# Kernel tuning notes

Hardware: AMD Instinct MI355X
Metric: run time of the kernel (lower is better)

The kernel has to match this reference:

```python
import jax, jax.numpy as jnp
import numpy as np

EPS = 1e-5


def _ln(t):
    # Custom LayerNorm from the source: unbiased variance (torch.var default),
    # gamma=ones, beta=zeros (plain tensors, never trained) -> plain normalize.
    m = t.mean(axis=-1, keepdims=True)
    v = t.var(axis=-1, keepdims=True, ddof=1)
    return (t - m) / jnp.sqrt(v + EPS)


def setup_inputs() -> dict:
    key = jax.random.key(0)
    B, T, C, H = 4, 2048, 1024, 16
    hs = C // H
    ks = jax.random.split(key, 10)
    s_in = (1.0 / C) ** 0.5   # nn.Linear default init scale (approx, uniform->normal ok for ref)
    s_ff = (1.0 / (4 * C)) ** 0.5
    return {
        "x": jax.random.normal(ks[0], (B, T, C), jnp.float32),
        "Wq": jax.random.normal(ks[1], (H, C, hs), jnp.float32) * s_in,
        "Wk": jax.random.normal(ks[2], (H, C, hs), jnp.float32) * s_in,
        "Wv": jax.random.normal(ks[3], (H, C, hs), jnp.float32) * s_in,
        "Wo": jax.random.normal(ks[4], (C, C), jnp.float32) * s_in,
        "bo": jnp.zeros((C,), jnp.float32),
        "W1": jax.random.normal(ks[5], (C, 4 * C), jnp.float32) * s_in,
        "b1": jnp.zeros((4 * C,), jnp.float32),
        "W2": jax.random.normal(ks[6], (4 * C, C), jnp.float32) * s_ff,
        "b2": jnp.zeros((C,), jnp.float32),
    }


def reference(x, Wq, Wk, Wv, Wo, bo, W1, b1, W2, b2):
    B, T, C = x.shape
    H, _, hs = Wq.shape
    # per-head projections (equivalent to the Python loop over Head modules)
    q = jnp.einsum('btc,hcd->bhtd', x, Wq)
    k = jnp.einsum('btc,hcd->bhtd', x, Wk)
    v = jnp.einsum('btc,hcd->bhtd', x, Wv)
    scores = jnp.einsum('bhtd,bhsd->bhts', q, k) * (hs ** -0.5)
    causal = jnp.tril(jnp.ones((T, T), dtype=bool))
    scores = jnp.where(causal, scores, jnp.float32(-jnp.inf))
    w = jax.nn.softmax(scores, axis=-1)          # dropout is identity in eval
    o = jnp.einsum('bhts,bhsd->bhtd', w, v)
    o = o.transpose(0, 2, 1, 3).reshape(B, T, C)  # concat heads
    attn = o @ Wo + bo
    x1 = x + _ln(attn)
    ff = jax.nn.relu(x1 @ W1 + b1) @ W2 + b2
    return x1 + _ln(ff)
```

## Files before the change

### kernel.cpp

```cpp
#include <hip/hip_runtime.h>
#include <hip/hip_bf16.h>

using bf16 = __hip_bfloat16;
typedef __attribute__((ext_vector_type(8))) short s8v;
typedef __attribute__((ext_vector_type(4))) float f4v;
typedef __attribute__((ext_vector_type(16))) float f16v;
typedef __attribute__((ext_vector_type(4))) unsigned int u4v;

#define QSCALE 0.18033688011112042f

__device__ __forceinline__ void gld_lds16(const void* g, void* l) {
  __builtin_amdgcn_global_load_lds(
      (const __attribute__((address_space(1))) void*)g,
      (__attribute__((address_space(3))) void*)l, 16, 0, 0);
}

__device__ __forceinline__ unsigned short bfbits(float f) {
  bf16 t = __float2bfloat16(f);
  return *reinterpret_cast<unsigned short*>(&t);
}

__device__ __forceinline__ unsigned int pk2(float lo, float hi) {
  return (unsigned int)bfbits(lo) | ((unsigned int)bfbits(hi) << 16);
}

__device__ __forceinline__ void lswap(unsigned int& a, unsigned int& b) {
  asm("v_permlane32_swap_b32 %0, %1" : "+v"(a), "+v"(b));
}

__global__ __launch_bounds__(256) void f32_to_bf16_k(const float* __restrict__ in,
                                                     bf16* __restrict__ out, size_t n) {
  const size_t i = ((size_t)blockIdx.x * 256 + threadIdx.x) * 4;
  if (i + 3 < n) {
    const float4 v = *(const float4*)(in + i);
    out[i + 0] = __float2bfloat16(v.x);
    out[i + 1] = __float2bfloat16(v.y);
    out[i + 2] = __float2bfloat16(v.z);
    out[i + 3] = __float2bfloat16(v.w);
  }
}

__global__ __launch_bounds__(256) void tr_to_bf16_k(const float* __restrict__ in,
                                                    bf16* __restrict__ out,
                                                    int R, int C,
                                                    size_t inb, size_t outb) {
  __shared__ float tile[32][33];
  in  += (size_t)blockIdx.z * inb;
  out += (size_t)blockIdx.z * outb;
  const int r0 = blockIdx.y * 32, c0 = blockIdx.x * 32;
  const int tx = threadIdx.x & 31, ty = threadIdx.x >> 5;
#pragma unroll
  for (int i = 0; i < 4; ++i)
    tile[ty + i * 8][tx] = in[(size_t)(r0 + ty + i * 8) * C + c0 + tx];
  __syncthreads();
#pragma unroll
  for (int i = 0; i < 4; ++i)
    out[(size_t)(c0 + ty + i * 8) * R + r0 + tx] = __float2bfloat16(tile[tx][ty + i * 8]);
}

template <int MODE>
__global__ __launch_bounds__(256, 2) void gemm_bt(const bf16* __restrict__ A,
                                                  const bf16* __restrict__ B,
                                                  const float* __restrict__ bias,
                                                  float* __restrict__ Cf,
                                                  bf16* __restrict__ Cb,
                                                  bf16* __restrict__ Vout,
                                                  int M, int N, int K) {
  __shared__ __attribute__((aligned(16))) bf16 As[128 * 32];
  __shared__ __attribute__((aligned(16))) bf16 Bs[128 * 32];
  const int tid  = threadIdx.x;
  const int wid  = tid >> 6;
  const int lane = tid & 63;
  const int quad = lane >> 4;
  const int l16  = lane & 15;
  const int bm = blockIdx.y * 128;
  const int bn = blockIdx.x * 128;
  const int wm = (wid >> 1) * 64;
  const int wn = (wid & 1) * 64;

  f4v acc[4][4];
#pragma unroll
  for (int i = 0; i < 4; ++i)
#pragma unroll
    for (int j = 0; j < 4; ++j) acc[i][j] = (f4v){0.f, 0.f, 0.f, 0.f};

  const bf16* Ag = A + (size_t)(bm + wid * 32 + (lane >> 2)) * K + (lane & 3) * 8;
  const bf16* Bg = B + (size_t)(bn + wid * 32 + (lane >> 2)) * K + (lane & 3) * 8;
  bf16* AsW = As + wid * 32 * 32;
  bf16* BsW = Bs + wid * 32 * 32;

  for (int k0 = 0; k0 < K; k0 += 32) {
    __syncthreads();
    gld_lds16(Ag,                  AsW);
    gld_lds16(Ag + (size_t)16 * K, AsW + 16 * 32);
    gld_lds16(Bg,                  BsW);
    gld_lds16(Bg + (size_t)16 * K, BsW + 16 * 32);
    Ag += 32; Bg += 32;
    __syncthreads();

    s8v af[4], bfr[4];
#pragma unroll
    for (int mi = 0; mi < 4; ++mi)
      af[mi] = *(const s8v*)(As + (wm + mi * 16 + l16) * 32 + quad * 8);
#pragma unroll
    for (int ni = 0; ni < 4; ++ni)
      bfr[ni] = *(const s8v*)(Bs + (wn + ni * 16 + l16) * 32 + quad * 8);
#pragma unroll
    for (int mi = 0; mi < 4; ++mi)
#pragma unroll
      for (int ni = 0; ni < 4; ++ni)
        acc[mi][ni] = __builtin_amdgcn_mfma_f32_16x16x32_bf16(af[mi], bfr[ni], acc[mi][ni], 0, 0, 0);
  }

  const size_t ldc = (size_t)N;
#pragma unroll
  for (int mi = 0; mi < 4; ++mi) {
#pragma unroll
    for (int ni = 0; ni < 4; ++ni) {
      const int col  = bn + wn + ni * 16 + l16;
      const int row0 = bm + wm + mi * 16 + quad * 4;
      if (MODE == 0) {
        if (col < 2048) {
          const float sc = (col < 1024) ? QSCALE : 1.0f;
#pragma unroll
          for (int r = 0; r < 4; ++r)
            Cb[(size_t)(row0 + r) * ldc + col] = __float2bfloat16(acc[mi][ni][r] * sc);
        } else {
          ushort4 pk;
          pk.x = bfbits(acc[mi][ni][0]);
          pk.y = bfbits(acc[mi][ni][1]);
          pk.z = bfbits(acc[mi][ni][2]);
          pk.w = bfbits(acc[mi][ni][3]);
          const int bb = row0 >> 11, t = row0 & 2047;
          *(ushort4*)&Vout[((size_t)(bb * 1024 + col - 2048)) * 2048 + t] = pk;
        }
      } else {
        const float bv = bias[col];
#pragma unroll
        for (int r = 0; r < 4; ++r) {
          const float v = acc[mi][ni][r] + bv;
          if (MODE == 1) Cf[(size_t)(row0 + r) * ldc + col] = v;
          else           Cb[(size_t)(row0 + r) * ldc + col] = __float2bfloat16(fmaxf(v, 0.f));
        }
      }
    }
  }
}

template <int MODE>
__global__ __launch_bounds__(512, 2) void gemm256(const bf16* __restrict__ A,
                                                  const bf16* __restrict__ B,
                                                  const float* __restrict__ bias,
                                                  float* __restrict__ Cf,
                                                  bf16* __restrict__ Cb,
                                                  bf16* __restrict__ Vout,
                                                  int M, int N, int K) {
  __shared__ __attribute__((aligned(16))) bf16 AS[2][256 * 64];
  __shared__ __attribute__((aligned(16))) bf16 BS[2][256 * 64];

  const int tid  = threadIdx.x;
  const int wid  = tid >> 6;
  const int lane = tid & 63;
  const int l16  = lane & 15;
  const int quad = lane >> 4;
  const int wm   = wid >> 2;
  const int wn   = wid & 3;

  const int gx  = gridDim.x;
  const int nwg = gx * gridDim.y;
  int lin = blockIdx.y * gx + blockIdx.x;
  lin = (lin & 7) * (nwg >> 3) + (lin >> 3);
  const int bm = (lin / gx) * 256;
  const int bn = (lin % gx) * 256;

  const int d0 = tid * 16;
  const int a0 = d0 ^ (((d0 >> 9) & 1) << 5);
  const int sr = a0 >> 7;
  const int scol = (a0 & 127) >> 1;
  const bf16* Asrc = A + (size_t)(bm + sr) * K + scol;
  const bf16* Bsrc = B + (size_t)(bn + sr) * K + scol;
  char* const AW0 = (char*)&AS[0][0] + wid * 1024;
  char* const AW1 = (char*)&AS[1][0] + wid * 1024;
  char* const BW0 = (char*)&BS[0][0] + wid * 1024;
  char* const BW1 = (char*)&BS[1][0] + wid * 1024;

  const int sq16 = (quad * 16) ^ (((l16 >> 2) & 1) << 5);
  const int rdA  = l16 * 128 + sq16;
  const int rdB  = (wn & 1) * 8192 + l16 * 128 + sq16;

#define STAGE2(dst, src) \
  do { gld_lds16((src), (dst)); gld_lds16((src) + (size_t)64 * K, (dst) + 8192); } while (0)

  f4v acc[8][4];
#pragma unroll
  for (int i = 0; i < 8; ++i)
#pragma unroll
    for (int j = 0; j < 4; ++j) acc[i][j] = (f4v){0.f, 0.f, 0.f, 0.f};

  const int NT = K >> 6;

  STAGE2(AW0,         Asrc);
  STAGE2(AW0 + 16384, Asrc + (size_t)128 * K);
  STAGE2(BW0,         Bsrc);
  STAGE2(BW0 + 16384, Bsrc + (size_t)128 * K);
  STAGE2(BW1,         Bsrc + 64);
  STAGE2(BW1 + 16384, Bsrc + (size_t)128 * K + 64);
  asm volatile("s_waitcnt vmcnt(4)" ::: "memory");
  asm volatile("s_barrier" ::: "memory");

  s8v bfrag[4][2];
  for (int u = 0; u < NT; ++u) {
    const int bsel = u & 1;
    const char* Ard = (char*)&AS[bsel][0] + wm * 16384 + rdA;
    const char* Brd = (char*)&BS[bsel][0] + (wn >> 1) * 16384 + rdB;
    char* const AWn = bsel ? AW0 : AW1;
    char* const BWc = bsel ? BW1 : BW0;
    const bf16* An = Asrc + (size_t)(u + 1) * 64;
    const bf16* Bn = Bsrc + (size_t)(u + 2) * 64;
#pragma unroll
    for (int p = 0; p < 4; ++p) {
      s8v afrag[2][2];
#pragma unroll
      for (int j = 0; j < 2; ++j)
#pragma unroll
        for (int kk = 0; kk < 2; ++kk)
          afrag[j][kk] = *(const s8v*)(Ard + (p * 2 + j) * 2048 + kk * 64);
      if (p == 0) {
#pragma unroll
        for (int nf = 0; nf < 4; ++nf)
#pragma unroll
          for (int kk = 0; kk < 2; ++kk)
            bfrag[nf][kk] = *(const s8v*)(Brd + nf * 2048 + kk * 64);
      }
      if (p == 0 && u + 1 < NT) STAGE2(AWn,         An);
      if (p == 1 && u + 1 < NT) STAGE2(AWn + 16384, An + (size_t)128 * K);
      if (p == 2 && u + 2 < NT) STAGE2(BWc,         Bn);
      if (p == 3 && u + 2 < NT) STAGE2(BWc + 16384, Bn + (size_t)128 * K);
      asm volatile("s_barrier" ::: "memory");
      asm volatile("s_waitcnt lgkmcnt(0)" ::: "memory");
      __builtin_amdgcn_sched_barrier(0);
      __builtin_amdgcn_s_setprio(1);
#pragma unroll
      for (int kk = 0; kk < 2; ++kk)
#pragma unroll
        for (int j = 0; j < 2; ++j)
#pragma unroll
          for (int nf = 0; nf < 4; ++nf)
            acc[p * 2 + j][nf] = __builtin_amdgcn_mfma_f32_16x16x32_bf16(
                afrag[j][kk], bfrag[nf][kk], acc[p * 2 + j][nf], 0, 0, 0);
      __builtin_amdgcn_s_setprio(0);
      if (p == 3) {
        if (u + 2 < NT) asm volatile("s_waitcnt vmcnt(4)" ::: "memory");
        else            asm volatile("s_waitcnt vmcnt(0)" ::: "memory");
      }
      asm volatile("s_barrier" ::: "memory");
    }
  }
#undef STAGE2

  const size_t ldc = (size_t)N;
#pragma unroll
  for (int mf = 0; mf < 8; ++mf) {
#pragma unroll
    for (int nf = 0; nf < 4; ++nf) {
      const int col  = bn + wn * 64 + nf * 16 + l16;
      const int row0 = bm + wm * 128 + mf * 16 + quad * 4;
      if (MODE == 0) {
        if (col < 2048) {
          const float sc = (col < 1024) ? QSCALE : 1.0f;
#pragma unroll
          for (int r = 0; r < 4; ++r)
            Cb[(size_t)(row0 + r) * ldc + col] = __float2bfloat16(acc[mf][nf][r] * sc);
        } else {
          ushort4 pk;
          pk.x = bfbits(acc[mf][nf][0]);
          pk.y = bfbits(acc[mf][nf][1]);
          pk.z = bfbits(acc[mf][nf][2]);
          pk.w = bfbits(acc[mf][nf][3]);
          const int bb = row0 >> 11, t = row0 & 2047;
          *(ushort4*)&Vout[((size_t)(bb * 1024 + col - 2048)) * 2048 + t] = pk;
        }
      } else {
        const float bv = bias[col];
#pragma unroll
        for (int r = 0; r < 4; ++r) {
          const float v = acc[mf][nf][r] + bv;
          if (MODE == 1) Cf[(size_t)(row0 + r) * ldc + col] = v;
          else           Cb[(size_t)(row0 + r) * ldc + col] = __float2bfloat16(fmaxf(v, 0.f));
        }
      }
    }
  }
}

__global__ __launch_bounds__(256, 3) void attn_mfma(const bf16* __restrict__ qkv,
                                                    const bf16* __restrict__ vtg,
                                                    bf16* __restrict__ o) {
  __shared__ __attribute__((aligned(16))) bf16 KsS[2][64 * 64];
  __shared__ __attribute__((aligned(16))) bf16 VtS[2][64 * 64];
  __shared__ __attribute__((aligned(16))) float tS[128];

  const int tid  = threadIdx.x;
  const int w    = tid >> 6;
  const int lane = tid & 63;
  const int l32  = lane & 31;
  const int hi   = lane >> 5;
  const int xq   = l32 & 7;

  const int lin = blockIdx.x;
  const int b = lin & 3;
  const int h = (lin >> 2) & 15;
  const int qt = 15 - (lin >> 6);

  const bf16* qbase = qkv + (size_t)b * 2048 * 3072 + h * 64;
  const bf16* kbase = qbase + 1024;
  const bf16* vbase = vtg + (size_t)(b * 1024 + h * 64) * 2048;

  const int rsub = lane >> 3;
  const int sseg = (lane & 7) ^ rsub;
  const int d0 = (w * 16) * 64;
  const int d1 = (w * 16 + 8) * 64;

  const int nkt = 2 * qt + 2;
  const int qmin_w = qt * 128 + w * 32;
  const int qmax_w = qmin_w + 31;
  const int q_lane = qmin_w + l32;

  s8v qf[4];
#pragma unroll
  for (int ks = 0; ks < 4; ++ks)
    qf[ks] = *(const s8v*)(qbase + (size_t)q_lane * 3072 + ks * 16 + hi * 8);

  float m_run = -1.0e38f, l_run = 0.f;
  f16v oacc[2];
#pragma unroll
  for (int dn = 0; dn < 2; ++dn)
#pragma unroll
    for (int r = 0; r < 16; ++r) oacc[dn][r] = 0.f;

  const bf16* kg = kbase + (size_t)(w * 16 + rsub) * 3072 + sseg * 8;
  const bf16* vg = vbase + (size_t)(w * 16 + rsub) * 2048 + sseg * 8;

  gld_lds16(kg,                    &KsS[0][d0]);
  gld_lds16(kg + (size_t)8 * 3072, &KsS[0][d1]);
  gld_lds16(vg,                    &VtS[0][d0]);
  gld_lds16(vg + (size_t)8 * 2048, &VtS[0][d1]);
  kg += (size_t)64 * 3072; vg += 64;
  __syncthreads();

  for (int kt = 0; kt < nkt; ++kt) {
    const int cb = kt & 1;

    if (kt + 1 < nkt) {
      const int nb = cb ^ 1;
      gld_lds16(kg,                    &KsS[nb][d0]);
      gld_lds16(kg + (size_t)8 * 3072, &KsS[nb][d1]);
      gld_lds16(vg,                    &VtS[nb][d0]);
      gld_lds16(vg + (size_t)8 * 2048, &VtS[nb][d1]);
      kg += (size_t)64 * 3072; vg += 64;
    }

    if (kt * 64 <= qmax_w) {
      const int kmmax = min(1, (qmax_w - kt * 64) >> 5);
      const bool diag = (kt * 64 + 63 > qmin_w);

      f16v sacc[2];
#pragma unroll
      for (int km = 0; km < 2; ++km)
#pragma unroll
        for (int r = 0; r < 16; ++r) sacc[km][r] = 0.f;

      for (int km = 0; km <= kmmax; ++km)
#pragma unroll
        for (int ks = 0; ks < 4; ++ks) {
          const s8v kf = *(const s8v*)&KsS[cb][(km * 32 + l32) * 64 +
                                               (((2 * ks + hi) ^ xq) << 3)];
          sacc[km] = __builtin_amdgcn_mfma_f32_32x32x16_bf16(kf, qf[ks], sacc[km], 0, 0, 0);
        }

      if (diag) {
        for (int km = 0; km <= kmmax; ++km)
#pragma unroll
          for (int r = 0; r < 16; ++r) {
            const int key = kt * 64 + km * 32 + (r & 3) + 8 * (r >> 2) + 4 * hi;
            if (key > q_lane) sacc[km][r] = -3.0e38f;
          }
      }

      float pmax = -3.0e38f;
#pragma unroll
      for (int km = 0; km < 2; ++km)
        if (km <= kmmax)
#pragma unroll
          for (int r = 0; r < 16; ++r) pmax = fmaxf(pmax, sacc[km][r]);
      pmax = fmaxf(pmax, __shfl_xor(pmax, 32));

      float mref = m_run;
      if (!__all(pmax <= m_run + 8.f)) {
        const float mnew = fmaxf(m_run, pmax);
        const float alpha = __builtin_amdgcn_exp2f(m_run - mnew);
        m_run = mnew; mref = mnew;
        l_run *= alpha;
        tS[w * 32 + l32] = alpha;
        f4v aF[4];
#pragma unroll
        for (int g = 0; g < 4; ++g)
          aF[g] = *(const f4v*)&tS[w * 32 + g * 8 + hi * 4];
#pragma unroll
        for (int dn = 0; dn < 2; ++dn)
#pragma unroll
          for (int r = 0; r < 16; ++r) oacc[dn][r] *= aF[r >> 2][r & 3];
      }

      float rs = 0.f;
      s8v pfr[4];
#pragma unroll
      for (int km = 0; km < 2; ++km)
        if (km <= kmmax) {
          float p[16];
#pragma unroll
          for (int r = 0; r < 16; ++r) {
            p[r] = __builtin_amdgcn_exp2f(sacc[km][r] - mref);
            rs += p[r];
          }
          unsigned int u0 = pk2(p[0], p[1]),  u1 = pk2(p[2], p[3]);
          unsigned int u2 = pk2(p[4], p[5]),  u3 = pk2(p[6], p[7]);
          lswap(u0, u2); lswap(u1, u3);
          u4v f0 = (u4v){u0, u1, u2, u3};
          pfr[2 * km] = *(s8v*)&f0;
          unsigned int v0 = pk2(p[8], p[9]),   v1 = pk2(p[10], p[11]);
          unsigned int v2 = pk2(p[12], p[13]), v3 = pk2(p[14], p[15]);
          lswap(v0, v2); lswap(v1, v3);
          u4v f1 = (u4v){v0, v1, v2, v3};
          pfr[2 * km + 1] = *(s8v*)&f1;
        }
      rs += __shfl_xor(rs, 32);
      l_run += rs;

#pragma unroll
      for (int ks = 0; ks < 4; ++ks)
        if ((ks >> 1) <= kmmax) {
#pragma unroll
          for (int dn = 0; dn < 2; ++dn) {
            const s8v vf = *(const s8v*)&VtS[cb][(dn * 32 + l32) * 64 +
                                                 (((2 * ks + hi) ^ xq) << 3)];
            oacc[dn] = __builtin_amdgcn_mfma_f32_32x32x16_bf16(pfr[ks], vf, oacc[dn], 0, 0, 0);
          }
        }
    }
    __syncthreads();
  }

  tS[w * 32 + l32] = l_run;
  f4v lF[4];
#pragma unroll
  for (int g = 0; g < 4; ++g)
    lF[g] = *(const f4v*)&tS[w * 32 + g * 8 + hi * 4];

#pragma unroll
  for (int r = 0; r < 16; ++r) {
    const float inv = __builtin_amdgcn_rcpf(lF[r >> 2][r & 3]);
    const int row = qt * 128 + w * 32 + (r & 3) + 8 * (r >> 2) + 4 * hi;
    bf16* dst = o + ((size_t)b * 2048 + row) * 1024 + h * 64 + l32;
    dst[0]  = __float2bfloat16(oacc[0][r] * inv);
    dst[32] = __float2bfloat16(oacc[1][r] * inv);
  }
}

__global__ __launch_bounds__(256) void ln_res(const float* __restrict__ xres,
                                              const float* __restrict__ t,
                                              float* __restrict__ xo,
                                              bf16* __restrict__ xob) {
  __shared__ float red[2][4];
  const int tid = threadIdx.x;
  const size_t base = (size_t)blockIdx.x * 1024;
  float v[4];
  float s = 0.f;
#pragma unroll
  for (int i = 0; i < 4; ++i) { v[i] = t[base + tid + i * 256]; s += v[i]; }
#pragma unroll
  for (int off = 32; off > 0; off >>= 1) s += __shfl_xor(s, off, 64);
  if ((tid & 63) == 0) red[0][tid >> 6] = s;
  __syncthreads();
  const float mean = (red[0][0] + red[0][1] + red[0][2] + red[0][3]) * (1.f / 1024.f);
  float ss = 0.f;
#pragma unroll
  for (int i = 0; i < 4; ++i) { const float d = v[i] - mean; ss += d * d; }
#pragma unroll
  for (int off = 32; off > 0; off >>= 1) ss += __shfl_xor(ss, off, 64);
  if ((tid & 63) == 0) red[1][tid >> 6] = ss;
  __syncthreads();
  const float var = (red[1][0] + red[1][1] + red[1][2] + red[1][3]) * (1.f / 1023.f);
  const float rstd = rsqrtf(var + 1e-5f);
#pragma unroll
  for (int i = 0; i < 4; ++i) {
    const size_t idx = base + tid + i * 256;
    const float r = xres[idx] + (v[i] - mean) * rstd;
    xo[idx] = r;
    if (xob) xob[idx] = __float2bfloat16(r);
  }
}

extern "C" void kernel_launch(void* const* d_in, const int* in_sizes, int n_in,
                              void* d_out, int out_size, void* d_ws, size_t ws_size,
                              hipStream_t stream) {
  const float* x  = (const float*)d_in[0];
  const float* Wq = (const float*)d_in[1];
  const float* Wk = (const float*)d_in[2];
  const float* Wv = (const float*)d_in[3];
  const float* Wo = (const float*)d_in[4];
  const float* bo = (const float*)d_in[5];
  const float* W1 = (const float*)d_in[6];
  const float* b1 = (const float*)d_in[7];
  const float* W2 = (const float*)d_in[8];
  const float* b2 = (const float*)d_in[9];
  float* out = (float*)d_out;

  char* ws = (char*)d_ws;
  bf16* qkv_bf = (bf16*)(ws);
  bf16* x_bf   = (bf16*)(ws + 50331648);
  bf16* WqkvT  = (bf16*)(ws + 67108864);
  bf16* WoT    = (bf16*)(ws + 73400320);
  bf16* W1T    = (bf16*)(ws + 75497472);
  bf16* W2T    = (bf16*)(ws + 83886080);
  bf16* o_bf   = (bf16*)(ws + 92274688);
  float* attn  = (float*)(ws + 109051904);
  float* x1    = (float*)(ws + 142606336);
  bf16* x1b    = (bf16*)(ws + 176160768);
  bf16* vt     = (bf16*)(ws + 192937984);
  bf16* h1     = (bf16*)(ws);
  float* ff    = (float*)(ws + 109051904);

  f32_to_bf16_k<<<8192, 256, 0, stream>>>(x, x_bf, (size_t)8388608);
  tr_to_bf16_k<<<dim3(2, 32, 16), 256, 0, stream>>>(Wq, WqkvT,               1024, 64,   65536, 65536);
  tr_to_bf16_k<<<dim3(2, 32, 16), 256, 0, stream>>>(Wk, WqkvT + 1024 * 1024, 1024, 64,   65536, 65536);
  tr_to_bf16_k<<<dim3(2, 32, 16), 256, 0, stream>>>(Wv, WqkvT + 2048 * 1024, 1024, 64,   65536, 65536);
  tr_to_bf16_k<<<dim3(32, 32, 1), 256, 0, stream>>>(Wo, WoT,                 1024, 1024, 0, 0);
  tr_to_bf16_k<<<dim3(128, 32, 1), 256, 0, stream>>>(W1, W1T,                1024, 4096, 0, 0);
  tr_to_bf16_k<<<dim3(32, 128, 1), 256, 0, stream>>>(W2, W2T,                4096, 1024, 0, 0);

  gemm256<0><<<dim3(12, 32), 512, 0, stream>>>(x_bf, WqkvT, nullptr, nullptr, qkv_bf, vt, 8192, 3072, 1024);

  attn_mfma<<<1024, 256, 0, stream>>>(qkv_bf, vt, o_bf);

  gemm_bt<1><<<dim3(8, 64), 256, 0, stream>>>(o_bf, WoT, bo, attn, nullptr, nullptr, 8192, 1024, 1024);

  ln_res<<<8192, 256, 0, stream>>>(x, attn, x1, x1b);

  gemm256<2><<<dim3(16, 32), 512, 0, stream>>>(x1b, W1T, b1, nullptr, h1, nullptr, 8192, 4096, 1024);
  gemm_bt<1><<<dim3(8, 64), 256, 0, stream>>>(h1, W2T, b2, ff, nullptr, nullptr, 8192, 1024, 4096);

  ln_res<<<8192, 256, 0, stream>>>(x1, ff, out, nullptr);
}
```

Before: 536.3 us.

## Template pipelined 256-row GEMM on N-tile and use it for N=1024 GEMMs

Makes the pipelined double-buffered 256-row GEMM generic over the N-tile width (256 or 128) and replaces the simple single-buffered 128x128 gemm_bt kernel for the Wo and W2 projections with a 256x128 instance. The intent is to bring the better software pipeline, LDS swizzle and larger M-tile to the N=1024 GEMMs, including the K=4096 FFN down-projection. The cost is fewer workgroups (256 instead of 512), which may under-fill the GPU's compute units and leave wave occupancy low.

Measured after the change: 509.8 us. 4.9% less time.

```diff
diff --git a/kernel.cpp b/kernel.cpp
--- a/kernel.cpp
+++ b/kernel.cpp
@@ -58,105 +58,18 @@
     out[(size_t)(c0 + ty + i * 8) * R + r0 + tx] = __float2bfloat16(tile[tx][ty + i * 8]);
 }
 
-template <int MODE>
-__global__ __launch_bounds__(256, 2) void gemm_bt(const bf16* __restrict__ A,
-                                                  const bf16* __restrict__ B,
-                                                  const float* __restrict__ bias,
-                                                  float* __restrict__ Cf,
-                                                  bf16* __restrict__ Cb,
-                                                  bf16* __restrict__ Vout,
-                                                  int M, int N, int K) {
-  __shared__ __attribute__((aligned(16))) bf16 As[128 * 32];
-  __shared__ __attribute__((aligned(16))) bf16 Bs[128 * 32];
-  const int tid  = threadIdx.x;
-  const int wid  = tid >> 6;
-  const int lane = tid & 63;
-  const int quad = lane >> 4;
-  const int l16  = lane & 15;
-  const int bm = blockIdx.y * 128;
-  const int bn = blockIdx.x * 128;
-  const int wm = (wid >> 1) * 64;
-  const int wn = (wid & 1) * 64;
-
-  f4v acc[4][4];
-#pragma unroll
-  for (int i = 0; i < 4; ++i)
-#pragma unroll
-    for (int j = 0; j < 4; ++j) acc[i][j] = (f4v){0.f, 0.f, 0.f, 0.f};
-
-  const bf16* Ag = A + (size_t)(bm + wid * 32 + (lane >> 2)) * K + (lane & 3) * 8;
-  const bf16* Bg = B + (size_t)(bn + wid * 32 + (lane >> 2)) * K + (lane & 3) * 8;
-  bf16* AsW = As + wid * 32 * 32;
-  bf16* BsW = Bs + wid * 32 * 32;
-
-  for (int k0 = 0; k0 < K; k0 += 32) {
-    __syncthreads();
-    gld_lds16(Ag,                  AsW);
-    gld_lds16(Ag + (size_t)16 * K, AsW + 16 * 32);
-    gld_lds16(Bg,                  BsW);
-    gld_lds16(Bg + (size_t)16 * K, BsW + 16 * 32);
-    Ag += 32; Bg += 32;
-    __syncthreads();
-
-    s8v af[4], bfr[4];
-#pragma unroll
-    for (int mi = 0; mi < 4; ++mi)
-      af[mi] = *(const s8v*)(As + (wm + mi * 16 + l16) * 32 + quad * 8);
-#pragma unroll
-    for (int ni = 0; ni < 4; ++ni)
-      bfr[ni] = *(const s8v*)(Bs + (wn + ni * 16 + l16) * 32 + quad * 8);
-#pragma unroll
-    for (int mi = 0; mi < 4; ++mi)
-#pragma unroll
-      for (int ni = 0; ni < 4; ++ni)
-        acc[mi][ni] = __builtin_amdgcn_mfma_f32_16x16x32_bf16(af[mi], bfr[ni], acc[mi][ni], 0, 0, 0);
-  }
-
-  const size_t ldc = (size_t)N;
-#pragma unroll
-  for (int mi = 0; mi < 4; ++mi) {
-#pragma unroll
-    for (int ni = 0; ni < 4; ++ni) {
-      const int col  = bn + wn + ni * 16 + l16;
-      const int row0 = bm + wm + mi * 16 + quad * 4;
-      if (MODE == 0) {
-        if (col < 2048) {
-          const float sc = (col < 1024) ? QSCALE : 1.0f;
-#pragma unroll
-          for (int r = 0; r < 4; ++r)
-            Cb[(size_t)(row0 + r) * ldc + col] = __float2bfloat16(acc[mi][ni][r] * sc);
-        } else {
-          ushort4 pk;
-          pk.x = bfbits(acc[mi][ni][0]);
-          pk.y = bfbits(acc[mi][ni][1]);
-          pk.z = bfbits(acc[mi][ni][2]);
-          pk.w = bfbits(acc[mi][ni][3]);
-          const int bb = row0 >> 11, t = row0 & 2047;
-          *(ushort4*)&Vout[((size_t)(bb * 1024 + col - 2048)) * 2048 + t] = pk;
-        }
-      } else {
-        const float bv = bias[col];
-#pragma unroll
-        for (int r = 0; r < 4; ++r) {
-          const float v = acc[mi][ni][r] + bv;
-          if (MODE == 1) Cf[(size_t)(row0 + r) * ldc + col] = v;
-          else           Cb[(size_t)(row0 + r) * ldc + col] = __float2bfloat16(fmaxf(v, 0.f));
-        }
-      }
-    }
-  }
-}
-
-template <int MODE>
-__global__ __launch_bounds__(512, 2) void gemm256(const bf16* __restrict__ A,
-                                                  const bf16* __restrict__ B,
-                                                  const float* __restrict__ bias,
-                                                  float* __restrict__ Cf,
-                                                  bf16* __restrict__ Cb,
-                                                  bf16* __restrict__ Vout,
-                                                  int M, int N, int K) {
+template <int MODE, int BN>
+__global__ __launch_bounds__(512, 2) void gemmT(const bf16* __restrict__ A,
+                                                const bf16* __restrict__ B,
+                                                const float* __restrict__ bias,
+                                                float* __restrict__ Cf,
+                                                bf16* __restrict__ Cb,
+                                                bf16* __restrict__ Vout,
+                                                int M, int N, int K) {
+  constexpr int NF = BN / 64;
+  constexpr int BH = BN / 128;
   __shared__ __attribute__((aligned(16))) bf16 AS[2][256 * 64];
-  __shared__ __attribute__((aligned(16))) bf16 BS[2][256 * 64];
+  __shared__ __attribute__((aligned(16))) bf16 BS[2][BN * 64];
 
   const int tid  = threadIdx.x;
   const int wid  = tid >> 6;
@@ -171,7 +84,7 @@
   int lin = blockIdx.y * gx + blockIdx.x;
   lin = (lin & 7) * (nwg >> 3) + (lin >> 3);
   const int bm = (lin / gx) * 256;
-  const int bn = (lin % gx) * 256;
+  const int bn = (lin % gx) * BN;
 
   const int d0 = tid * 16;
   const int a0 = d0 ^ (((d0 >> 9) & 1) << 5);
@@ -186,33 +99,39 @@
 
   const int sq16 = (quad * 16) ^ (((l16 >> 2) & 1) << 5);
   const int rdA  = l16 * 128 + sq16;
-  const int rdB  = (wn & 1) * 8192 + l16 * 128 + sq16;
-
-#define STAGE2(dst, src) \
+  const int rdB  = wn * (BN / 4) * 128 + l16 * 128 + sq16;
+
+#define STAGE_A2(dst, src) \
   do { gld_lds16((src), (dst)); gld_lds16((src) + (size_t)64 * K, (dst) + 8192); } while (0)
-
-  f4v acc[8][4];
+#define STAGE_BH(dst, src) \
+  do { gld_lds16((src), (dst)); \
+       if constexpr (BH == 2) gld_lds16((src) + (size_t)64 * K, (dst) + 8192); } while (0)
+#define WAIT_B_INFLIGHT() \
+  do { if constexpr (BN == 256) asm volatile("s_waitcnt vmcnt(4)" ::: "memory"); \
+       else                     asm volatile("s_waitcnt vmcnt(2)" ::: "memory"); } while (0)
+
+  f4v acc[8][NF];
 #pragma unroll
   for (int i = 0; i < 8; ++i)
 #pragma unroll
-    for (int j = 0; j < 4; ++j) acc[i][j] = (f4v){0.f, 0.f, 0.f, 0.f};
+    for (int j = 0; j < NF; ++j) acc[i][j] = (f4v){0.f, 0.f, 0.f, 0.f};
 
   const int NT = K >> 6;
 
-  STAGE2(AW0,         Asrc);
-  STAGE2(AW0 + 16384, Asrc + (size_t)128 * K);
-  STAGE2(BW0,         Bsrc);
-  STAGE2(BW0 + 16384, Bsrc + (size_t)128 * K);
-  STAGE2(BW1,         Bsrc + 64);
-  STAGE2(BW1 + 16384, Bsrc + (size_t)128 * K + 64);
-  asm volatile("s_waitcnt vmcnt(4)" ::: "memory");
+  STAGE_A2(AW0,         Asrc);
+  STAGE_A2(AW0 + 16384, Asrc + (size_t)128 * K);
+  STAGE_BH(BW0,             Bsrc);
+  STAGE_BH(BW0 + BH * 8192, Bsrc + (size_t)(BH * 64) * K);
+  STAGE_BH(BW1,             Bsrc + 64);
+  STAGE_BH(BW1 + BH * 8192, Bsrc + (size_t)(BH * 64) * K + 64);
+  WAIT_B_INFLIGHT();
   asm volatile("s_barrier" ::: "memory");
 
-  s8v bfrag[4][2];
+  s8v bfrag[NF][2];
   for (int u = 0; u < NT; ++u) {
     const int bsel = u & 1;
     const char* Ard = (char*)&AS[bsel][0] + wm * 16384 + rdA;
-    const char* Brd = (char*)&BS[bsel][0] + (wn >> 1) * 16384 + rdB;
+    const char* Brd = (char*)&BS[bsel][0] + rdB;
     char* const AWn = bsel ? AW0 : AW1;
     char* const BWc = bsel ? BW1 : BW0;
     const bf16* An = Asrc + (size_t)(u + 1) * 64;
@@ -227,15 +146,15 @@
           afrag[j][kk] = *(const s8v*)(Ard + (p * 2 + j) * 2048 + kk * 64);
       if (p == 0) {
 #pragma unroll
-        for (int nf = 0; nf < 4; ++nf)
+        for (int nf = 0; nf < NF; ++nf)
 #pragma unroll
           for (int kk = 0; kk < 2; ++kk)
             bfrag[nf][kk] = *(const s8v*)(Brd + nf * 2048 + kk * 64);
       }
-      if (p == 0 && u + 1 < NT) STAGE2(AWn,         An);
-      if (p == 1 && u + 1 < NT) STAGE2(AWn + 16384, An + (size_t)128 * K);
-      if (p == 2 && u + 2 < NT) STAGE2(BWc,         Bn);
-      if (p == 3 && u + 2 < NT) STAGE2(BWc + 16384, Bn + (size_t)128 * K);
+      if (p == 0 && u + 1 < NT) STAGE_A2(AWn,         An);
+      if (p == 1 && u + 1 < NT) STAGE_A2(AWn + 16384, An + (size_t)128 * K);
+      if (p == 2 && u + 2 < NT) STAGE_BH(BWc,             Bn);
+      if (p == 3 && u + 2 < NT) STAGE_BH(BWc + BH * 8192, Bn + (size_t)(BH * 64) * K);
       asm volatile("s_barrier" ::: "memory");
       asm volatile("s_waitcnt lgkmcnt(0)" ::: "memory");
       __builtin_amdgcn_sched_barrier(0);
@@ -245,25 +164,27 @@
 #pragma unroll
         for (int j = 0; j < 2; ++j)
 #pragma unroll
-          for (int nf = 0; nf < 4; ++nf)
+          for (int nf = 0; nf < NF; ++nf)
             acc[p * 2 + j][nf] = __builtin_amdgcn_mfma_f32_16x16x32_bf16(
                 afrag[j][kk], bfrag[nf][kk], acc[p * 2 + j][nf], 0, 0, 0);
       __builtin_amdgcn_s_setprio(0);
       if (p == 3) {
-        if (u + 2 < NT) asm volatile("s_waitcnt vmcnt(4)" ::: "memory");
+        if (u + 2 < NT) WAIT_B_INFLIGHT();
         else            asm volatile("s_waitcnt vmcnt(0)" ::: "memory");
       }
       asm volatile("s_barrier" ::: "memory");
     }
   }
-#undef STAGE2
+#undef STAGE_A2
+#undef STAGE_BH
+#undef WAIT_B_INFLIGHT
 
   const size_t ldc = (size_t)N;
 #pragma unroll
   for (int mf = 0; mf < 8; ++mf) {
 #pragma unroll
-    for (int nf = 0; nf < 4; ++nf) {
-      const int col  = bn + wn * 64 + nf * 16 + l16;
+    for (int nf = 0; nf < NF; ++nf) {
+      const int col  = bn + wn * (BN / 4) + nf * 16 + l16;
       const int row0 = bm + wm * 128 + mf * 16 + quad * 4;
       if (MODE == 0) {
         if (col < 2048) {
@@ -539,16 +460,17 @@
   tr_to_bf16_k<<<dim3(128, 32, 1), 256, 0, stream>>>(W1, W1T,                1024, 4096, 0, 0);
   tr_to_bf16_k<<<dim3(32, 128, 1), 256, 0, stream>>>(W2, W2T,                4096, 1024, 0, 0);
 
-  gemm256<0><<<dim3(12, 32), 512, 0, stream>>>(x_bf, WqkvT, nullptr, nullptr, qkv_bf, vt, 8192, 3072, 1024);
+  gemmT<0, 256><<<dim3(12, 32), 512, 0, stream>>>(x_bf, WqkvT, nullptr, nullptr, qkv_bf, vt, 8192, 3072, 1024);
 
   attn_mfma<<<1024, 256, 0, stream>>>(qkv_bf, vt, o_bf);
 
-  gemm_bt<1><<<dim3(8, 64), 256, 0, stream>>>(o_bf, WoT, bo, attn, nullptr, nullptr, 8192, 1024, 1024);
+  gemmT<1, 128><<<dim3(8, 32), 512, 0, stream>>>(o_bf, WoT, bo, attn, nullptr, nullptr, 8192, 1024, 1024);
 
   ln_res<<<8192, 256, 0, stream>>>(x, attn, x1, x1b);
 
-  gemm256<2><<<dim3(16, 32), 512, 0, stream>>>(x1b, W1T, b1, nullptr, h1, nullptr, 8192, 4096, 1024);
-  gemm_bt<1><<<dim3(8, 64), 256, 0, stream>>>(h1, W2T, b2, ff, nullptr, nullptr, 8192, 1024, 4096);
+  gemmT<2, 256><<<dim3(16, 32), 512, 0, stream>>>(x1b, W1T, b1, nullptr, h1, nullptr, 8192, 4096, 1024);
+
+  gemmT<1, 128><<<dim3(8, 32), 512, 0, stream>>>(h1, W2T, b2, ff, nullptr, nullptr, 8192, 1024, 4096);
 
   ln_res<<<8192, 256, 0, stream>>>(x1, ff, out, nullptr);
 }
```
